# Kernel tuning notes

Measured on AMD Instinct MI355X. Metric: run time of the kernel, lower is better.

## Reference

```python
import jax, jax.numpy as jnp
import numpy as np

B, L, H = 4, 2048, 1024
NQ, NKV, D = 8, 2, 256
I, V = 3584, 16384
EPS = 1e-6
THETA = 1e7
ROPE_DIM = 64

def rmsnorm(x, w, eps=EPS):
    xf = x.astype(jnp.float32)
    rms = jax.lax.rsqrt(jnp.mean(xf * xf, axis=-1, keepdims=True) + eps)
    return (xf * rms).astype(x.dtype) * w

def apply_rope(x, positions):
    # x: [B, H, L, D]; rotate first ROPE_DIM dims, interleaved pairs
    n_pairs = ROPE_DIM // 2
    inv_freq = THETA ** (-2.0 * jnp.arange(n_pairs, dtype=jnp.float32) / ROPE_DIM)
    freqs = positions.astype(jnp.float32)[:, None] * inv_freq[None, :]  # [L, n_pairs]
    cos = jnp.cos(freqs)[None, None, :, :]
    sin = jnp.sin(freqs)[None, None, :, :]
    b, h, l, d = x.shape
    xr = x[..., :ROPE_DIM].reshape(b, h, l, n_pairs, 2)
    x0, x1 = xr[..., 0], xr[..., 1]
    r0 = x0 * cos - x1 * sin
    r1 = x0 * sin + x1 * cos
    rotated = jnp.stack([r0, r1], axis=-1).reshape(b, h, l, ROPE_DIM)
    return jnp.concatenate([rotated, x[..., ROPE_DIM:]], axis=-1)

def setup_inputs() -> dict:
    key = jax.random.key(0)
    ks = jax.random.split(key, 12)
    s = 0.02
    return {
        "embeddings": jax.random.normal(ks[0], (B, L, H), jnp.float32),
        "hidden_states": jax.random.normal(ks[1], (B, L, H), jnp.float32),
        "pre_emb_w": jnp.ones((H,), jnp.float32),
        "pre_hid_w": jnp.ones((H,), jnp.float32),
        "fc_w": jax.random.normal(ks[2], (H, 2 * H), jnp.float32) * s,
        "in_ln_w": jnp.ones((H,), jnp.float32),
        "q_w": jax.random.normal(ks[3], (2 * NQ * D, H), jnp.float32) * s,
        "k_w": jax.random.normal(ks[4], (NKV * D, H), jnp.float32) * s,
        "v_w": jax.random.normal(ks[5], (NKV * D, H), jnp.float32) * s,
        "o_w": jax.random.normal(ks[6], (H, NQ * D), jnp.float32) * s,
        "qn_w": jnp.ones((D,), jnp.float32),
        "kn_w": jnp.ones((D,), jnp.float32),
        "post_ln_w": jnp.ones((H,), jnp.float32),
        "gate_w": jax.random.normal(ks[7], (I, H), jnp.float32) * s,
        "up_w": jax.random.normal(ks[8], (I, H), jnp.float32) * s,
        "down_w": jax.random.normal(ks[9], (H, I), jnp.float32) * s,
        "norm_w": jnp.ones((H,), jnp.float32),
        "lm_w": jax.random.normal(ks[10], (V, H), jnp.float32) * s,
    }

def _attention(x, q_w, k_w, v_w, o_w, qn_w, kn_w):
    b, l, _ = x.shape
    qg = (x @ q_w.T).reshape(b, l, NQ, 2, D)
    q = qg[:, :, :, 0, :]
    gate = qg[:, :, :, 1, :]
    k = (x @ k_w.T).reshape(b, l, NKV, D)
    v = (x @ v_w.T).reshape(b, l, NKV, D)
    q = rmsnorm(q, qn_w)
    k = rmsnorm(k, kn_w)
    groups = NQ // NKV
    k = jnp.repeat(k, groups, axis=2)  # [B, L, NQ, D]
    v = jnp.repeat(v, groups, axis=2)
    q, k, v = (t.transpose(0, 2, 1, 3) for t in (q, k, v))  # [B, NQ, L, D]
    positions = jnp.arange(l)
    q = apply_rope(q, positions)
    k = apply_rope(k, positions)
    scores = jnp.einsum('bhqd,bhkd->bhqk', q, k) / jnp.sqrt(jnp.float32(D))
    causal = jnp.tril(jnp.ones((l, l), jnp.bool_))
    scores = jnp.where(causal[None, None], scores, jnp.finfo(scores.dtype).min)
    attn = jax.nn.softmax(scores, axis=-1)
    out = jnp.einsum('bhqk,bhkd->bhqd', attn, v)
    out = out.transpose(0, 2, 1, 3).reshape(b, l, NQ * D)
    out = out * jax.nn.sigmoid(gate.reshape(b, l, NQ * D))
    return out @ o_w.T

def reference(embeddings, hidden_states, pre_emb_w, pre_hid_w, fc_w, in_ln_w,
              q_w, k_w, v_w, o_w, qn_w, kn_w, post_ln_w, gate_w, up_w, down_w,
              norm_w, lm_w):
    x = jnp.concatenate([rmsnorm(embeddings, pre_emb_w),
                         rmsnorm(hidden_states, pre_hid_w)], axis=-1)
    x = x @ fc_w.T
    residual = x
    x = rmsnorm(x, in_ln_w)
    x = _attention(x, q_w, k_w, v_w, o_w, qn_w, kn_w)
    x = residual + x
    residual = x
    x = rmsnorm(x, post_ln_w)
    x = (jax.nn.silu(x @ gate_w.T) * (x @ up_w.T)) @ down_w.T
    x = residual + x
    x = rmsnorm(x, norm_w)
    return x @ lm_w.T
```

## Files before the change

### kernel.cpp

```cpp
#include <hip/hip_runtime.h>

typedef __bf16 bf16;
typedef __bf16 bf16x8 __attribute__((ext_vector_type(8)));
typedef __bf16 bf16x4 __attribute__((ext_vector_type(4)));
typedef float f32x4 __attribute__((ext_vector_type(4)));

__device__ inline f32x4 mfma16(bf16x8 a, bf16x8 b, f32x4 c) {
    return __builtin_amdgcn_mfma_f32_16x16x32_bf16(a, b, c, 0, 0, 0);
}

__device__ __forceinline__ void async_cp16(const void* g, void* l) {
    __builtin_amdgcn_global_load_lds(
        (__attribute__((address_space(1))) char*)g,
        (__attribute__((address_space(3))) char*)l,
        16, 0, 0);
}

__global__ __launch_bounds__(256) void w2b_kernel(const float* __restrict__ s,
                                                  bf16* __restrict__ d)
{
    const size_t i = ((size_t)blockIdx.x * 256 + threadIdx.x) * 4;
    const float4 f = *(const float4*)(s + i);
    bf16x4 t;
    t[0] = (bf16)f.x; t[1] = (bf16)f.y; t[2] = (bf16)f.z; t[3] = (bf16)f.w;
    *(bf16x4*)(d + i) = t;
}

template <int EPI>
__global__ __launch_bounds__(256) void gemm_kernel(
    const bf16* __restrict__ A, const bf16* __restrict__ B,
    const float* __restrict__ res, float* __restrict__ Cout,
    int M, int N, int K)
{
    __shared__ bf16 As[128 * 32];
    __shared__ bf16 Bs[128 * 32];
    const int tid = threadIdx.x;
    const int wave = tid >> 6, lane = tid & 63;
    const int quad = lane >> 4, l16 = lane & 15;

    const int nby = M >> 7, nbx = N >> 7;
    const int nwg = nbx * nby;
    int bid = blockIdx.x;
    {
        const int q = nwg >> 3, r = nwg & 7;
        const int x = bid & 7, loc = bid >> 3;
        bid = (x < r ? x * (q + 1) : r * (q + 1) + (x - r) * q) + loc;
    }
    const int pg = nbx << 3;
    const int g = bid / pg, rem = bid - g * pg;
    const int by = (g << 3) + (rem & 7);
    const int bx = rem >> 3;
    const int row0 = by << 7, col0 = bx << 7;
    const int wrow = ((wave >> 1) << 6), wcol = ((wave & 1) << 6);

    f32x4 acc[4][4] = {};

    const bf16* Ag = A + (size_t)(row0 + (tid >> 2)) * K + (tid & 3) * 8;
    const bf16* Bg = B + (size_t)(col0 + (tid >> 2)) * K + (tid & 3) * 8;
    bf16* Asw = As + wave * 512;
    bf16* Bsw = Bs + wave * 512;
    const size_t K64 = (size_t)64 * K;

    for (int kb = 0; kb < K; kb += 32) {
        async_cp16(Ag + kb,        Asw);
        async_cp16(Ag + K64 + kb,  Asw + 2048);
        async_cp16(Bg + kb,        Bsw);
        async_cp16(Bg + K64 + kb,  Bsw + 2048);
        __syncthreads();
        bf16x8 af[4], bfr[4];
#pragma unroll
        for (int i = 0; i < 4; ++i)
            af[i] = *(const bf16x8*)(&As[(wrow + i * 16 + l16) * 32 + quad * 8]);
#pragma unroll
        for (int j = 0; j < 4; ++j)
            bfr[j] = *(const bf16x8*)(&Bs[(wcol + j * 16 + l16) * 32 + quad * 8]);
#pragma unroll
        for (int i = 0; i < 4; ++i)
#pragma unroll
            for (int j = 0; j < 4; ++j)
                acc[i][j] = mfma16(af[i], bfr[j], acc[i][j]);
        __syncthreads();
    }

#pragma unroll
    for (int i = 0; i < 4; ++i) {
        const int row = row0 + wrow + i * 16 + quad * 4;
#pragma unroll
        for (int j = 0; j < 4; ++j) {
            const int col = col0 + wcol + j * 16 + l16;
#pragma unroll
            for (int r = 0; r < 4; ++r) {
                const size_t idx = (size_t)(row + r) * N + col;
                float v = acc[i][j][r];
                if (EPI == 1) Cout[idx] = v + res[idx];
                else          Cout[idx] = v;
            }
        }
    }
}

template <int EPI>
__global__ __launch_bounds__(512, 2) void gemm256_kernel(
    const bf16* __restrict__ A, const bf16* __restrict__ B,
    const float* __restrict__ res, float* __restrict__ Cout,
    bf16* __restrict__ hout, int M, int N, int K)
{
    __shared__ bf16 As[2][2][128][64];
    __shared__ bf16 Bs[2][2][128][64];
    const int tid = threadIdx.x;
    const int wid = tid >> 6, lane = tid & 63;
    const int quad = lane >> 4, l16 = lane & 15;
    const int wm = wid >> 2, wn = wid & 3;
    const int xsw = l16 & 7;
    const int bofs = (wn & 1) * 64;

    const int nby = M >> 8, nbx = N >> 8;
    const int nwg = nbx * nby;
    int bid = blockIdx.x;
    {
        const int q = nwg >> 3, r = nwg & 7;
        const int x = bid & 7, loc = bid >> 3;
        bid = (x < r ? x * (q + 1) : r * (q + 1) + (x - r) * q) + loc;
    }
    const int pg = nbx << 3;
    const int g = bid / pg, rem = bid - g * pg;
    const int by = (g << 3) + (rem & 7);
    const int bx = rem >> 3;
    const int row0 = by << 8, col0 = bx << 8;

    const int srow = tid >> 3;
    const int scol = ((tid & 7) ^ ((tid >> 3) & 7)) * 8;
    const bf16* Abase = A + (size_t)(row0 + srow) * K + scol;
    const bf16* Bbase = B + (size_t)(col0 + srow) * K + scol;
    const size_t K64 = (size_t)K * 64;
    const size_t K128 = (size_t)K * 128;

    f32x4 acc[8][4] = {};
    bf16x8 af[8], bf0[4], bf1[4];

#define STG_A(BUF, HH, KB) do { \
    const bf16* _g = Abase + (size_t)(HH) * K128 + (KB); \
    bf16* _l = &As[BUF][HH][0][0] + wid * 512; \
    async_cp16(_g, _l); \
    async_cp16(_g + K64, _l + 4096); } while (0)
#define STG_B(BUF, HH, KB) do { \
    const bf16* _g = Bbase + (size_t)(HH) * K128 + (KB); \
    bf16* _l = &Bs[BUF][HH][0][0] + wid * 512; \
    async_cp16(_g, _l); \
    async_cp16(_g + K64, _l + 4096); } while (0)

#define RD_A(BUF, RH) do { \
    const bf16 (*Ah_)[64] = As[BUF][wm]; \
    _Pragma("unroll") for (int f = 0; f < 4; ++f) { \
        af[f*2+0] = *(const bf16x8*)(&Ah_[(RH)*64 + f*16 + l16][(quad ^ xsw) * 8]); \
        af[f*2+1] = *(const bf16x8*)(&Ah_[(RH)*64 + f*16 + l16][((4 + quad) ^ xsw) * 8]); } } while (0)

#define RD_B(BUF, CH, BF) do { \
    const bf16 (*Bh_)[64] = Bs[BUF][wn >> 1]; \
    _Pragma("unroll") for (int f = 0; f < 2; ++f) { \
        BF[f*2+0] = *(const bf16x8*)(&Bh_[bofs + (CH)*32 + f*16 + l16][(quad ^ xsw) * 8]); \
        BF[f*2+1] = *(const bf16x8*)(&Bh_[bofs + (CH)*32 + f*16 + l16][((4 + quad) ^ xsw) * 8]); } } while (0)

#define MFMA_Q(RH, CH, BF) do { \
    _Pragma("unroll") for (int f = 0; f < 4; ++f) \
    _Pragma("unroll") for (int f2 = 0; f2 < 2; ++f2) { \
        acc[(RH)*4+f][(CH)*2+f2] = mfma16(af[f*2+0], BF[f2*2+0], acc[(RH)*4+f][(CH)*2+f2]); \
        acc[(RH)*4+f][(CH)*2+f2] = mfma16(af[f*2+1], BF[f2*2+1], acc[(RH)*4+f][(CH)*2+f2]); } } while (0)

    const int NT = K >> 6;
    STG_A(0, 0, 0); STG_A(0, 1, 0); STG_B(0, 0, 0); STG_B(0, 1, 0);
    if (NT > 1) {
        STG_A(1, 0, 64); STG_A(1, 1, 64); STG_B(1, 0, 64); STG_B(1, 1, 64);
        asm volatile("s_waitcnt vmcnt(8)" ::: "memory");
    } else {
        asm volatile("s_waitcnt vmcnt(0)" ::: "memory");
    }
    __builtin_amdgcn_sched_barrier(0);
    __builtin_amdgcn_s_barrier();
    RD_A(0, 0); RD_B(0, 0, bf0); RD_B(0, 1, bf1);
    __builtin_amdgcn_sched_barrier(0);

    for (int t = 0; t < NT; ++t) {
        const int c = t & 1, n = c ^ 1;
        const int kb1 = (t + 1) << 6, kb2 = (t + 2) << 6;
        if (t >= 1 && t + 1 < NT) { STG_A(n, 0, kb1); STG_A(n, 1, kb1); }
        asm volatile("s_waitcnt lgkmcnt(4)" ::: "memory");
        __builtin_amdgcn_sched_barrier(0);
        __builtin_amdgcn_s_setprio(1);
        MFMA_Q(0, 0, bf0);
        __builtin_amdgcn_s_setprio(0);
        asm volatile("s_waitcnt lgkmcnt(0)" ::: "memory");
        __builtin_amdgcn_sched_barrier(0);
        __builtin_amdgcn_s_setprio(1);
        MFMA_Q(0, 1, bf1);
        __builtin_amdgcn_s_setprio(0);
        RD_A(c, 1);
        __builtin_amdgcn_sched_barrier(0);
        __builtin_amdgcn_s_barrier();
        if (t + 2 < NT) { STG_B(c, 0, kb2); STG_B(c, 1, kb2); }
        asm volatile("s_waitcnt lgkmcnt(0)" ::: "memory");
        __builtin_amdgcn_sched_barrier(0);
        __builtin_amdgcn_s_setprio(1);
        MFMA_Q(1, 0, bf0);
        MFMA_Q(1, 1, bf1);
        __builtin_amdgcn_s_setprio(0);
        if (t + 1 < NT) {
            if (t + 2 < NT) { asm volatile("s_waitcnt vmcnt(4)" ::: "memory"); }
            else            { asm volatile("s_waitcnt vmcnt(0)" ::: "memory"); }
            __builtin_amdgcn_sched_barrier(0);
            RD_A(n, 0); RD_B(n, 0, bf0); RD_B(n, 1, bf1);
            __builtin_amdgcn_sched_barrier(0);
        }
        __builtin_amdgcn_s_barrier();
    }
#undef STG_A
#undef STG_B
#undef RD_A
#undef RD_B
#undef MFMA_Q

#pragma unroll
    for (int fr = 0; fr < 8; ++fr) {
        const int row = row0 + wm * 128 + fr * 16 + quad * 4;
#pragma unroll
        for (int fc = 0; fc < 4; ++fc) {
            const int col = col0 + wn * 64 + fc * 16 + l16;
#pragma unroll
            for (int r = 0; r < 4; ++r) {
                const size_t idx = (size_t)(row + r) * N + col;
                float v = acc[fr][fc][r];
                if (EPI == 1) {
                    Cout[idx] = v + res[idx];
                } else if (EPI == 2) {
                    const float gg = res[idx];
                    hout[idx] = (bf16)(gg * (1.f / (1.f + __expf(-gg))) * v);
                } else {
                    Cout[idx] = v;
                }
            }
        }
    }
}

__global__ __launch_bounds__(256) void prenorm_kernel(
    const float* __restrict__ emb, const float* __restrict__ hid,
    const float* __restrict__ we, const float* __restrict__ wh,
    bf16* __restrict__ xcat)
{
    const int rr = blockIdx.x * 4 + (threadIdx.x >> 6);
    const int lane = threadIdx.x & 63;
    const int half = rr & 1, row = rr >> 1;
    const float* x = (half ? hid : emb) + (size_t)row * 1024;
    const float* w = half ? wh : we;
    float4 v[4]; float ss = 0.f;
#pragma unroll
    for (int j = 0; j < 4; ++j) {
        v[j] = *(const float4*)(x + (size_t)(lane + 64 * j) * 4);
        ss += v[j].x * v[j].x + v[j].y * v[j].y + v[j].z * v[j].z + v[j].w * v[j].w;
    }
#pragma unroll
    for (int m = 32; m; m >>= 1) ss += __shfl_xor(ss, m, 64);
    const float rms = rsqrtf(ss * (1.f / 1024.f) + 1e-6f);
    bf16* o = xcat + (size_t)row * 2048 + half * 1024;
#pragma unroll
    for (int j = 0; j < 4; ++j) {
        const int d = (lane + 64 * j) * 4;
        float4 wv = *(const float4*)(w + d);
        bf16x4 t;
        t[0] = (bf16)(v[j].x * rms * wv.x);
        t[1] = (bf16)(v[j].y * rms * wv.y);
        t[2] = (bf16)(v[j].z * rms * wv.z);
        t[3] = (bf16)(v[j].w * rms * wv.w);
        *(bf16x4*)(o + d) = t;
    }
}

__global__ __launch_bounds__(256) void rmsnorm_kernel(
    const float* __restrict__ xin, const float* __restrict__ w, bf16* __restrict__ out)
{
    const int row = blockIdx.x * 4 + (threadIdx.x >> 6);
    const int lane = threadIdx.x & 63;
    const float* x = xin + (size_t)row * 1024;
    float4 v[4]; float ss = 0.f;
#pragma unroll
    for (int j = 0; j < 4; ++j) {
        v[j] = *(const float4*)(x + (size_t)(lane + 64 * j) * 4);
        ss += v[j].x * v[j].x + v[j].y * v[j].y + v[j].z * v[j].z + v[j].w * v[j].w;
    }
#pragma unroll
    for (int m = 32; m; m >>= 1) ss += __shfl_xor(ss, m, 64);
    const float rms = rsqrtf(ss * (1.f / 1024.f) + 1e-6f);
    bf16* o = out + (size_t)row * 1024;
#pragma unroll
    for (int j = 0; j < 4; ++j) {
        const int d = (lane + 64 * j) * 4;
        float4 wv = *(const float4*)(w + d);
        bf16x4 t;
        t[0] = (bf16)(v[j].x * rms * wv.x);
        t[1] = (bf16)(v[j].y * rms * wv.y);
        t[2] = (bf16)(v[j].z * rms * wv.z);
        t[3] = (bf16)(v[j].w * rms * wv.w);
        *(bf16x4*)(o + d) = t;
    }
}

__global__ __launch_bounds__(256) void qprep_kernel(
    const float* __restrict__ qg, const float* __restrict__ qn_w, bf16* __restrict__ qa)
{
    const int row = blockIdx.x * 4 + (threadIdx.x >> 6);
    const int lane = threadIdx.x & 63;
    const int h = row & 7, bl = row >> 3;
    const int l = bl & 2047, b = bl >> 11;
    const float* x = qg + (size_t)row * 512;
    float v[4]; float ss = 0.f;
#pragma unroll
    for (int j = 0; j < 4; ++j) { v[j] = x[lane + 64 * j]; ss += v[j] * v[j]; }
#pragma unroll
    for (int m = 32; m; m >>= 1) ss += __shfl_xor(ss, m, 64);
    const float rms = rsqrtf(ss * (1.f / 256.f) + 1e-6f);
    float y[4];
#pragma unroll
    for (int j = 0; j < 4; ++j) y[j] = v[j] * rms * qn_w[lane + 64 * j];
    {
        const float p = __shfl_xor(y[0], 1, 64);
        const int i2 = lane >> 1;
        const float inv = powf(1e7f, -(float)(2 * i2) * (1.f / 64.f));
        const float ang = (float)l * inv;
        const float c = cosf(ang), s = sinf(ang);
        y[0] = (lane & 1) ? (p * s + y[0] * c) : (y[0] * c - p * s);
    }
    bf16* o = qa + ((size_t)((b * 8 + h) * 2048 + l)) * 256;
#pragma unroll
    for (int j = 0; j < 4; ++j) o[lane + 64 * j] = (bf16)(y[j] * 0.0625f);
}

__global__ __launch_bounds__(256) void kprep_kernel(
    const float* __restrict__ kf, const float* __restrict__ kn_w, bf16* __restrict__ ka)
{
    const int row = blockIdx.x * 4 + (threadIdx.x >> 6);
    const int lane = threadIdx.x & 63;
    const int kv = row & 1, bl = row >> 1;
    const int l = bl & 2047, b = bl >> 11;
    const float* x = kf + (size_t)row * 256;
    float v[4]; float ss = 0.f;
#pragma unroll
    for (int j = 0; j < 4; ++j) { v[j] = x[lane + 64 * j]; ss += v[j] * v[j]; }
#pragma unroll
    for (int m = 32; m; m >>= 1) ss += __shfl_xor(ss, m, 64);
    const float rms = rsqrtf(ss * (1.f / 256.f) + 1e-6f);
    float y[4];
#pragma unroll
    for (int j = 0; j < 4; ++j) y[j] = v[j] * rms * kn_w[lane + 64 * j];
    {
        const float p = __shfl_xor(y[0], 1, 64);
        const int i2 = lane >> 1;
        const float inv = powf(1e7f, -(float)(2 * i2) * (1.f / 64.f));
        const float ang = (float)l * inv;
        const float c = cosf(ang), s = sinf(ang);
        y[0] = (lane & 1) ? (p * s + y[0] * c) : (y[0] * c - p * s);
    }
    bf16* o = ka + ((size_t)((b * 2 + kv) * 2048 + l)) * 256;
#pragma unroll
    for (int j = 0; j < 4; ++j) o[lane + 64 * j] = (bf16)y[j];
}

__global__ __launch_bounds__(256) void vprep_kernel(const float* __restrict__ vf,
                                                    bf16* __restrict__ vt)
{
    __shared__ float t[64][65];
    const int l0 = blockIdx.x << 6;
    const int d0 = blockIdx.y << 6;
    const int b = blockIdx.z >> 1, kv = blockIdx.z & 1;
    const int tx = threadIdx.x & 63, ty = threadIdx.x >> 6;
    const float* src = vf + ((size_t)b * 4096 + kv) * 256;
#pragma unroll
    for (int j = 0; j < 16; ++j) {
        const int l = ty + j * 4;
        t[l][tx] = src[(size_t)(l0 + l) * 512 + d0 + tx];
    }
    __syncthreads();
    bf16* dst = vt + (size_t)(b * 2 + kv) * 256 * 2048;
#pragma unroll
    for (int j = 0; j < 16; ++j) {
        const int d = ty + j * 4;
        dst[(size_t)(d0 + d) * 2048 + l0 + tx] = (bf16)t[tx][d];
    }
}

__global__ __launch_bounds__(256) void attn_kernel(
    const bf16* __restrict__ qa, const bf16* __restrict__ ka,
    const bf16* __restrict__ vt, const float* __restrict__ qg,
    bf16* __restrict__ ag)
{
    __shared__ bf16 Ks[32 * 264];
    __shared__ bf16 Vt[256 * 40];
    __shared__ bf16 Pw[4 * 16 * 40];
    const int tid = threadIdx.x;
    const int wave = tid >> 6, lane = tid & 63;
    const int quad = lane >> 4, l16 = lane & 15;
    const int bid = blockIdx.x;
    const int j = bid & 15, h = (bid >> 4) & 7, b = bid >> 7;
    const int kvh = h >> 2;
    const bf16* qptr = qa + ((size_t)(b * 8 + h)) * 2048 * 256;
    const bf16* kptr = ka + ((size_t)(b * 2 + kvh)) * 2048 * 256;
    const bf16* vptr = vt + ((size_t)(b * 2 + kvh)) * 256 * 2048;

    for (int s = 0; s < 2; ++s) {
        const int qt = s ? (31 - j) : j;
        const int qbase = qt * 64 + wave * 16;

        bf16x8 qf[8];
#pragma unroll
        for (int db = 0; db < 8; ++db)
            qf[db] = *(const bf16x8*)(qptr + (size_t)(qbase + l16) * 256 + db * 32 + quad * 8);

        f32x4 o_acc[16] = {};
        float m_i[4], l_i[4];
#pragma unroll
        for (int r = 0; r < 4; ++r) { m_i[r] = -1e30f; l_i[r] = 0.f; }

        const int ntiles = qt * 2 + 2;
        for (int kt = 0; kt < ntiles; ++kt) {
            const int kvs = kt * 32;
#pragma unroll
            for (int c = 0; c < 4; ++c) {
                const int idx = tid + c * 256;
                const int kr = idx >> 5, kc = (idx & 31) * 8;
                *(bf16x8*)(&Ks[kr * 264 + kc]) = *(const bf16x8*)(kptr + (size_t)(kvs + kr) * 256 + kc);
                const int vd = idx >> 2, vc = (idx & 3) * 8;
                *(bf16x8*)(&Vt[vd * 40 + vc]) = *(const bf16x8*)(vptr + (size_t)vd * 2048 + kvs + vc);
            }
            __syncthreads();

            f32x4 s0 = {}, s1 = {};
#pragma unroll
            for (int db = 0; db < 8; ++db) {
                bf16x8 k0 = *(const bf16x8*)(&Ks[l16 * 264 + db * 32 + quad * 8]);
                bf16x8 k1 = *(const bf16x8*)(&Ks[(16 + l16) * 264 + db * 32 + quad * 8]);
                s0 = mfma16(qf[db], k0, s0);
                s1 = mfma16(qf[db], k1, s1);
            }

            float alpha[4], p0v[4], p1v[4];
#pragma unroll
            for (int r = 0; r < 4; ++r) {
                const int qrow = qbase + quad * 4 + r;
                float a0 = (kvs + l16 > qrow) ? -1e30f : s0[r];
                float a1 = (kvs + 16 + l16 > qrow) ? -1e30f : s1[r];
                float mx = fmaxf(a0, a1);
#pragma unroll
                for (int m = 8; m; m >>= 1) mx = fmaxf(mx, __shfl_xor(mx, m, 64));
                const float mnew = fmaxf(m_i[r], mx);
                const float a = __expf(m_i[r] - mnew);
                const float p0 = __expf(a0 - mnew);
                const float p1 = __expf(a1 - mnew);
                float ps = p0 + p1;
#pragma unroll
                for (int m = 8; m; m >>= 1) ps += __shfl_xor(ps, m, 64);
                l_i[r] = l_i[r] * a + ps;
                m_i[r] = mnew;
                alpha[r] = a; p0v[r] = p0; p1v[r] = p1;
            }
#pragma unroll
            for (int t = 0; t < 16; ++t) {
                f32x4 o = o_acc[t];
                o[0] *= alpha[0]; o[1] *= alpha[1]; o[2] *= alpha[2]; o[3] *= alpha[3];
                o_acc[t] = o;
            }
            bf16* pw = &Pw[wave * 16 * 40];
#pragma unroll
            for (int r = 0; r < 4; ++r) {
                pw[(quad * 4 + r) * 40 + l16]      = (bf16)p0v[r];
                pw[(quad * 4 + r) * 40 + 16 + l16] = (bf16)p1v[r];
            }
            __syncthreads();
            const bf16x8 pa = *(const bf16x8*)(&pw[l16 * 40 + quad * 8]);
#pragma unroll
            for (int t = 0; t < 16; ++t) {
                bf16x8 vfr = *(const bf16x8*)(&Vt[(t * 16 + l16) * 40 + quad * 8]);
                o_acc[t] = mfma16(pa, vfr, o_acc[t]);
            }
            __syncthreads();
        }

#pragma unroll
        for (int r = 0; r < 4; ++r) {
            const float inv = 1.f / l_i[r];
            const int row = qbase + quad * 4 + r;
            const float* gr = qg + ((size_t)((b * 2048 + row) * 8 + h)) * 512 + 256;
            bf16* ar = ag + ((size_t)(b * 2048 + row)) * 2048 + h * 256;
#pragma unroll
            for (int t = 0; t < 16; ++t) {
                const int d = t * 16 + l16;
                const float o = o_acc[t][r] * inv;
                const float gg = gr[d];
                ar[d] = (bf16)(o * (1.f / (1.f + __expf(-gg))));
            }
        }
    }
}

extern "C" void kernel_launch(void* const* d_in, const int* in_sizes, int n_in,
                              void* d_out, int out_size, void* d_ws, size_t ws_size,
                              hipStream_t stream)
{
    const float* emb       = (const float*)d_in[0];
    const float* hid       = (const float*)d_in[1];
    const float* pre_emb_w = (const float*)d_in[2];
    const float* pre_hid_w = (const float*)d_in[3];
    const float* fc_w      = (const float*)d_in[4];
    const float* in_ln_w   = (const float*)d_in[5];
    const float* q_w       = (const float*)d_in[6];
    const float* k_w       = (const float*)d_in[7];
    const float* v_w       = (const float*)d_in[8];
    const float* o_w       = (const float*)d_in[9];
    const float* qn_w      = (const float*)d_in[10];
    const float* kn_w      = (const float*)d_in[11];
    const float* post_ln_w = (const float*)d_in[12];
    const float* gate_w    = (const float*)d_in[13];
    const float* up_w      = (const float*)d_in[14];
    const float* down_w    = (const float*)d_in[15];
    const float* norm_w    = (const float*)d_in[16];
    const float* lm_w      = (const float*)d_in[17];
    float* out = (float*)d_out;
    char* ws = (char*)d_ws;

    float* xres = (float*)(ws + 0);
    bf16*  xln  = (bf16*)(ws + 33554432);
    char*  C    = ws + 50331648;
    char*  D    = ws + 184549376;
    char*  E    = ws + 318767104;
    float* qg   = (float*)C;
    float* gf   = (float*)C;
    bf16*  xcat = (bf16*)D;
    float* kf   = (float*)(D + 33554432);
    float* vf   = (float*)(D + 50331648);
    bf16*  ag   = (bf16*)(D + 67108864);
    bf16*  qa   = (bf16*)E;
    bf16*  ka   = (bf16*)(E + 33554432);
    bf16*  va   = (bf16*)(E + 41943040);
    bf16*  hb   = (bf16*)E;
    bf16*  wbC  = (bf16*)C;
    bf16*  wbD  = (bf16*)D;
    bf16*  wbDt = (bf16*)(D + 117440512);

    prenorm_kernel<<<4096, 256, 0, stream>>>(emb, hid, pre_emb_w, pre_hid_w, xcat);

    w2b_kernel<<<2048, 256, 0, stream>>>(fc_w, wbC);
    gemm_kernel<0><<<512, 256, 0, stream>>>(xcat, wbC, nullptr, xres, 8192, 1024, 2048);
    rmsnorm_kernel<<<2048, 256, 0, stream>>>(xres, in_ln_w, xln);

    w2b_kernel<<<4096, 256, 0, stream>>>(q_w, wbD);
    gemm256_kernel<0><<<512, 512, 0, stream>>>(xln, wbD, nullptr, qg, nullptr, 8192, 4096, 1024);
    w2b_kernel<<<512, 256, 0, stream>>>(k_w, wbD);
    gemm_kernel<0><<<256, 256, 0, stream>>>(xln, wbD, nullptr, kf, 8192, 512, 1024);
    w2b_kernel<<<512, 256, 0, stream>>>(v_w, wbD);
    gemm_kernel<0><<<256, 256, 0, stream>>>(xln, wbD, nullptr, vf, 8192, 512, 1024);

    qprep_kernel<<<16384, 256, 0, stream>>>(qg, qn_w, qa);
    kprep_kernel<<<4096, 256, 0, stream>>>(kf, kn_w, ka);
    vprep_kernel<<<dim3(32, 4, 8), 256, 0, stream>>>(vf, va);
    attn_kernel<<<512, 256, 0, stream>>>(qa, ka, va, qg, ag);

    w2b_kernel<<<2048, 256, 0, stream>>>(o_w, wbC);
    gemm_kernel<1><<<512, 256, 0, stream>>>(ag, wbC, xres, xres, 8192, 1024, 2048);
    rmsnorm_kernel<<<2048, 256, 0, stream>>>(xres, post_ln_w, xln);

    w2b_kernel<<<3584, 256, 0, stream>>>(gate_w, wbDt);
    gemm256_kernel<0><<<448, 512, 0, stream>>>(xln, wbDt, nullptr, gf, nullptr, 8192, 3584, 1024);
    w2b_kernel<<<3584, 256, 0, stream>>>(up_w, wbDt);
    gemm256_kernel<2><<<448, 512, 0, stream>>>(xln, wbDt, gf, nullptr, hb, 8192, 3584, 1024);

    w2b_kernel<<<3584, 256, 0, stream>>>(down_w, wbC);
    gemm_kernel<1><<<512, 256, 0, stream>>>(hb, wbC, xres, xres, 8192, 1024, 3584);
    rmsnorm_kernel<<<2048, 256, 0, stream>>>(xres, norm_w, xln);

    w2b_kernel<<<16384, 256, 0, stream>>>(lm_w, wbC);
    gemm256_kernel<0><<<2048, 512, 0, stream>>>(xln, wbC, nullptr, out, nullptr, 8192, 16384, 1024);
}
```

Before: 1.787 ms.

## Widen GEMM K-tile with swizzled LDS, merge K/V GEMM, batch weight casts, vectorize prep

The 128x128 GEMM now stages 64-wide K tiles into XOR-swizzled LDS. This halves the loop iterations and barriers, and the swizzle is meant to avoid bank conflicts. The K and V projections are merged into a single GEMM whose output is an interleaved KV buffer, and the weight casts for q/k/v and gate/up are each batched into one launch. The q/k prep kernels use float4 loads and compute RoPE on contiguous pairs inside a lane instead of using shuffles. This cuts launch count and instruction overhead, at the cost of more LDS per block and changed indexing.

```diff
diff --git a/kernel.cpp b/kernel.cpp
--- a/kernel.cpp
+++ b/kernel.cpp
@@ -26,17 +26,48 @@
     *(bf16x4*)(d + i) = t;
 }
 
+__global__ __launch_bounds__(256) void w2b_qkv_kernel(
+    const float* __restrict__ qw, const float* __restrict__ kw,
+    const float* __restrict__ vw, bf16* __restrict__ dq)
+{
+    int bid = blockIdx.x;
+    const float* s; bf16* d;
+    if (bid < 4096)      { s = qw; d = dq; }
+    else if (bid < 4608) { s = kw; d = dq + 4194304; bid -= 4096; }
+    else                 { s = vw; d = dq + 4718592; bid -= 4608; }
+    const size_t i = ((size_t)bid * 256 + threadIdx.x) * 4;
+    const float4 f = *(const float4*)(s + i);
+    bf16x4 t;
+    t[0] = (bf16)f.x; t[1] = (bf16)f.y; t[2] = (bf16)f.z; t[3] = (bf16)f.w;
+    *(bf16x4*)(d + i) = t;
+}
+
+__global__ __launch_bounds__(256) void w2b_gu_kernel(
+    const float* __restrict__ gw, const float* __restrict__ uw, bf16* __restrict__ dg)
+{
+    int bid = blockIdx.x;
+    const float* s; bf16* d;
+    if (bid < 3584) { s = gw; d = dg; }
+    else            { s = uw; d = dg + 3670016; bid -= 3584; }
+    const size_t i = ((size_t)bid * 256 + threadIdx.x) * 4;
+    const float4 f = *(const float4*)(s + i);
+    bf16x4 t;
+    t[0] = (bf16)f.x; t[1] = (bf16)f.y; t[2] = (bf16)f.z; t[3] = (bf16)f.w;
+    *(bf16x4*)(d + i) = t;
+}
+
 template <int EPI>
 __global__ __launch_bounds__(256) void gemm_kernel(
     const bf16* __restrict__ A, const bf16* __restrict__ B,
     const float* __restrict__ res, float* __restrict__ Cout,
     int M, int N, int K)
 {
-    __shared__ bf16 As[128 * 32];
-    __shared__ bf16 Bs[128 * 32];
+    __shared__ bf16 As[128][64];
+    __shared__ bf16 Bs[128][64];
     const int tid = threadIdx.x;
     const int wave = tid >> 6, lane = tid & 63;
     const int quad = lane >> 4, l16 = lane & 15;
+    const int xsw = l16 & 7;
 
     const int nby = M >> 7, nbx = N >> 7;
     const int nwg = nbx * nby;
@@ -55,30 +86,37 @@
 
     f32x4 acc[4][4] = {};
 
-    const bf16* Ag = A + (size_t)(row0 + (tid >> 2)) * K + (tid & 3) * 8;
-    const bf16* Bg = B + (size_t)(col0 + (tid >> 2)) * K + (tid & 3) * 8;
-    bf16* Asw = As + wave * 512;
-    bf16* Bsw = Bs + wave * 512;
-    const size_t K64 = (size_t)64 * K;
-
-    for (int kb = 0; kb < K; kb += 32) {
-        async_cp16(Ag + kb,        Asw);
-        async_cp16(Ag + K64 + kb,  Asw + 2048);
-        async_cp16(Bg + kb,        Bsw);
-        async_cp16(Bg + K64 + kb,  Bsw + 2048);
+    const int srow = tid >> 3;
+    const int scol = ((tid & 7) ^ (srow & 7)) * 8;
+    const bf16* Ag = A + (size_t)(row0 + srow) * K + scol;
+    const bf16* Bg = B + (size_t)(col0 + srow) * K + scol;
+    const size_t K32 = (size_t)32 * K;
+
+    for (int kb = 0; kb < K; kb += 64) {
+#pragma unroll
+        for (int q = 0; q < 4; ++q) {
+            async_cp16(Ag + q * K32 + kb, &As[0][0] + q * 2048 + wave * 512);
+            async_cp16(Bg + q * K32 + kb, &Bs[0][0] + q * 2048 + wave * 512);
+        }
         __syncthreads();
-        bf16x8 af[4], bfr[4];
+        bf16x8 af[8], bfr[8];
+#pragma unroll
+        for (int i = 0; i < 4; ++i) {
+            af[i * 2 + 0] = *(const bf16x8*)(&As[wrow + i * 16 + l16][(quad ^ xsw) * 8]);
+            af[i * 2 + 1] = *(const bf16x8*)(&As[wrow + i * 16 + l16][((4 + quad) ^ xsw) * 8]);
+        }
+#pragma unroll
+        for (int j = 0; j < 4; ++j) {
+            bfr[j * 2 + 0] = *(const bf16x8*)(&Bs[wcol + j * 16 + l16][(quad ^ xsw) * 8]);
+            bfr[j * 2 + 1] = *(const bf16x8*)(&Bs[wcol + j * 16 + l16][((4 + quad) ^ xsw) * 8]);
+        }
 #pragma unroll
         for (int i = 0; i < 4; ++i)
-            af[i] = *(const bf16x8*)(&As[(wrow + i * 16 + l16) * 32 + quad * 8]);
-#pragma unroll
-        for (int j = 0; j < 4; ++j)
-            bfr[j] = *(const bf16x8*)(&Bs[(wcol + j * 16 + l16) * 32 + quad * 8]);
-#pragma unroll
-        for (int i = 0; i < 4; ++i)
-#pragma unroll
-            for (int j = 0; j < 4; ++j)
-                acc[i][j] = mfma16(af[i], bfr[j], acc[i][j]);
+#pragma unroll
+            for (int j = 0; j < 4; ++j) {
+                acc[i][j] = mfma16(af[i * 2 + 0], bfr[j * 2 + 0], acc[i][j]);
+                acc[i][j] = mfma16(af[i * 2 + 1], bfr[j * 2 + 1], acc[i][j]);
+            }
         __syncthreads();
     }
 
@@ -312,59 +350,62 @@
     const int h = row & 7, bl = row >> 3;
     const int l = bl & 2047, b = bl >> 11;
     const float* x = qg + (size_t)row * 512;
-    float v[4]; float ss = 0.f;
-#pragma unroll
-    for (int j = 0; j < 4; ++j) { v[j] = x[lane + 64 * j]; ss += v[j] * v[j]; }
+    float4 v = *(const float4*)(x + lane * 4);
+    float ss = v.x * v.x + v.y * v.y + v.z * v.z + v.w * v.w;
 #pragma unroll
     for (int m = 32; m; m >>= 1) ss += __shfl_xor(ss, m, 64);
     const float rms = rsqrtf(ss * (1.f / 256.f) + 1e-6f);
-    float y[4];
-#pragma unroll
-    for (int j = 0; j < 4; ++j) y[j] = v[j] * rms * qn_w[lane + 64 * j];
-    {
-        const float p = __shfl_xor(y[0], 1, 64);
-        const int i2 = lane >> 1;
-        const float inv = powf(1e7f, -(float)(2 * i2) * (1.f / 64.f));
-        const float ang = (float)l * inv;
-        const float c = cosf(ang), s = sinf(ang);
-        y[0] = (lane & 1) ? (p * s + y[0] * c) : (y[0] * c - p * s);
-    }
-    bf16* o = qa + ((size_t)((b * 8 + h) * 2048 + l)) * 256;
-#pragma unroll
-    for (int j = 0; j < 4; ++j) o[lane + 64 * j] = (bf16)(y[j] * 0.0625f);
+    const float4 wv = *(const float4*)(qn_w + lane * 4);
+    float y0 = v.x * rms * wv.x, y1 = v.y * rms * wv.y;
+    float y2 = v.z * rms * wv.z, y3 = v.w * rms * wv.w;
+    if (lane < 16) {
+        const float inv0 = powf(1e7f, -(float)(4 * lane) * (1.f / 64.f));
+        const float inv1 = powf(1e7f, -(float)(4 * lane + 2) * (1.f / 64.f));
+        const float a0 = (float)l * inv0, a1 = (float)l * inv1;
+        const float c0 = cosf(a0), s0 = sinf(a0), c1 = cosf(a1), s1 = sinf(a1);
+        const float r0 = y0 * c0 - y1 * s0, r1 = y0 * s0 + y1 * c0;
+        const float r2 = y2 * c1 - y3 * s1, r3 = y2 * s1 + y3 * c1;
+        y0 = r0; y1 = r1; y2 = r2; y3 = r3;
+    }
+    bf16* o = qa + ((size_t)((b * 8 + h) * 2048 + l)) * 256 + lane * 4;
+    bf16x4 t;
+    t[0] = (bf16)(y0 * 0.0625f); t[1] = (bf16)(y1 * 0.0625f);
+    t[2] = (bf16)(y2 * 0.0625f); t[3] = (bf16)(y3 * 0.0625f);
+    *(bf16x4*)o = t;
 }
 
 __global__ __launch_bounds__(256) void kprep_kernel(
-    const float* __restrict__ kf, const float* __restrict__ kn_w, bf16* __restrict__ ka)
+    const float* __restrict__ kvf, const float* __restrict__ kn_w, bf16* __restrict__ ka)
 {
     const int row = blockIdx.x * 4 + (threadIdx.x >> 6);
     const int lane = threadIdx.x & 63;
     const int kv = row & 1, bl = row >> 1;
     const int l = bl & 2047, b = bl >> 11;
-    const float* x = kf + (size_t)row * 256;
-    float v[4]; float ss = 0.f;
-#pragma unroll
-    for (int j = 0; j < 4; ++j) { v[j] = x[lane + 64 * j]; ss += v[j] * v[j]; }
+    const float* x = kvf + (size_t)bl * 1024 + kv * 256;
+    float4 v = *(const float4*)(x + lane * 4);
+    float ss = v.x * v.x + v.y * v.y + v.z * v.z + v.w * v.w;
 #pragma unroll
     for (int m = 32; m; m >>= 1) ss += __shfl_xor(ss, m, 64);
     const float rms = rsqrtf(ss * (1.f / 256.f) + 1e-6f);
-    float y[4];
-#pragma unroll
-    for (int j = 0; j < 4; ++j) y[j] = v[j] * rms * kn_w[lane + 64 * j];
-    {
-        const float p = __shfl_xor(y[0], 1, 64);
-        const int i2 = lane >> 1;
-        const float inv = powf(1e7f, -(float)(2 * i2) * (1.f / 64.f));
-        const float ang = (float)l * inv;
-        const float c = cosf(ang), s = sinf(ang);
-        y[0] = (lane & 1) ? (p * s + y[0] * c) : (y[0] * c - p * s);
-    }
-    bf16* o = ka + ((size_t)((b * 2 + kv) * 2048 + l)) * 256;
-#pragma unroll
-    for (int j = 0; j < 4; ++j) o[lane + 64 * j] = (bf16)y[j];
-}
-
-__global__ __launch_bounds__(256) void vprep_kernel(const float* __restrict__ vf,
+    const float4 wv = *(const float4*)(kn_w + lane * 4);
+    float y0 = v.x * rms * wv.x, y1 = v.y * rms * wv.y;
+    float y2 = v.z * rms * wv.z, y3 = v.w * rms * wv.w;
+    if (lane < 16) {
+        const float inv0 = powf(1e7f, -(float)(4 * lane) * (1.f / 64.f));
+        const float inv1 = powf(1e7f, -(float)(4 * lane + 2) * (1.f / 64.f));
+        const float a0 = (float)l * inv0, a1 = (float)l * inv1;
+        const float c0 = cosf(a0), s0 = sinf(a0), c1 = cosf(a1), s1 = sinf(a1);
+        const float r0 = y0 * c0 - y1 * s0, r1 = y0 * s0 + y1 * c0;
+        const float r2 = y2 * c1 - y3 * s1, r3 = y2 * s1 + y3 * c1;
+        y0 = r0; y1 = r1; y2 = r2; y3 = r3;
+    }
+    bf16* o = ka + ((size_t)((b * 2 + kv) * 2048 + l)) * 256 + lane * 4;
+    bf16x4 t;
+    t[0] = (bf16)y0; t[1] = (bf16)y1; t[2] = (bf16)y2; t[3] = (bf16)y3;
+    *(bf16x4*)o = t;
+}
+
+__global__ __launch_bounds__(256) void vprep_kernel(const float* __restrict__ kvf,
                                                     bf16* __restrict__ vt)
 {
     __shared__ float t[64][65];
@@ -372,11 +413,11 @@
     const int d0 = blockIdx.y << 6;
     const int b = blockIdx.z >> 1, kv = blockIdx.z & 1;
     const int tx = threadIdx.x & 63, ty = threadIdx.x >> 6;
-    const float* src = vf + ((size_t)b * 4096 + kv) * 256;
+    const float* src = kvf + (size_t)b * 2048 * 1024 + 512 + kv * 256;
 #pragma unroll
     for (int j = 0; j < 16; ++j) {
         const int l = ty + j * 4;
-        t[l][tx] = src[(size_t)(l0 + l) * 512 + d0 + tx];
+        t[l][tx] = src[(size_t)(l0 + l) * 1024 + d0 + tx];
     }
     __syncthreads();
     bf16* dst = vt + (size_t)(b * 2 + kv) * 256 * 2048;
@@ -533,8 +574,7 @@
     float* qg   = (float*)C;
     float* gf   = (float*)C;
     bf16*  xcat = (bf16*)D;
-    float* kf   = (float*)(D + 33554432);
-    float* vf   = (float*)(D + 50331648);
+    float* kvf  = (float*)(D + 33554432);
     bf16*  ag   = (bf16*)(D + 67108864);
     bf16*  qa   = (bf16*)E;
     bf16*  ka   = (bf16*)(E + 33554432);
@@ -542,6 +582,7 @@
     bf16*  hb   = (bf16*)E;
     bf16*  wbC  = (bf16*)C;
     bf16*  wbD  = (bf16*)D;
+    bf16*  wkv  = (bf16*)D + 4194304;
     bf16*  wbDt = (bf16*)(D + 117440512);
 
     prenorm_kernel<<<4096, 256, 0, stream>>>(emb, hid, pre_emb_w, pre_hid_w, xcat);
@@ -550,26 +591,22 @@
     gemm_kernel<0><<<512, 256, 0, stream>>>(xcat, wbC, nullptr, xres, 8192, 1024, 2048);
     rmsnorm_kernel<<<2048, 256, 0, stream>>>(xres, in_ln_w, xln);
 
-    w2b_kernel<<<4096, 256, 0, stream>>>(q_w, wbD);
+    w2b_qkv_kernel<<<5120, 256, 0, stream>>>(q_w, k_w, v_w, wbD);
     gemm256_kernel<0><<<512, 512, 0, stream>>>(xln, wbD, nullptr, qg, nullptr, 8192, 4096, 1024);
-    w2b_kernel<<<512, 256, 0, stream>>>(k_w, wbD);
-    gemm_kernel<0><<<256, 256, 0, stream>>>(xln, wbD, nullptr, kf, 8192, 512, 1024);
-    w2b_kernel<<<512, 256, 0, stream>>>(v_w, wbD);
-    gemm_kernel<0><<<256, 256, 0, stream>>>(xln, wbD, nullptr, vf, 8192, 512, 1024);
+    gemm_kernel<0><<<512, 256, 0, stream>>>(xln, wkv, nullptr, kvf, 8192, 1024, 1024);
 
     qprep_kernel<<<16384, 256, 0, stream>>>(qg, qn_w, qa);
-    kprep_kernel<<<4096, 256, 0, stream>>>(kf, kn_w, ka);
-    vprep_kernel<<<dim3(32, 4, 8), 256, 0, stream>>>(vf, va);
+    kprep_kernel<<<4096, 256, 0, stream>>>(kvf, kn_w, ka);
+    vprep_kernel<<<dim3(32, 4, 8), 256, 0, stream>>>(kvf, va);
     attn_kernel<<<512, 256, 0, stream>>>(qa, ka, va, qg, ag);
 
     w2b_kernel<<<2048, 256, 0, stream>>>(o_w, wbC);
     gemm_kernel<1><<<512, 256, 0, stream>>>(ag, wbC, xres, xres, 8192, 1024, 2048);
     rmsnorm_kernel<<<2048, 256, 0, stream>>>(xres, post_ln_w, xln);
 
-    w2b_kernel<<<3584, 256, 0, stream>>>(gate_w, wbDt);
+    w2b_gu_kernel<<<7168, 256, 0, stream>>>(gate_w, up_w, wbDt);
     gemm256_kernel<0><<<448, 512, 0, stream>>>(xln, wbDt, nullptr, gf, nullptr, 8192, 3584, 1024);
-    w2b_kernel<<<3584, 256, 0, stream>>>(up_w, wbDt);
-    gemm256_kernel<2><<<448, 512, 0, stream>>>(xln, wbDt, gf, nullptr, hb, 8192, 3584, 1024);
+    gemm256_kernel<2><<<448, 512, 0, stream>>>(xln, wbDt + 3670016, gf, nullptr, hb, 8192, 3584, 1024);
 
     w2b_kernel<<<3584, 256, 0, stream>>>(down_w, wbC);
     gemm_kernel<1><<<512, 256, 0, stream>>>(hb, wbC, xres, xres, 8192, 1024, 3584);
```

Result: faster. 1.728 ms (-3.3%).
